# Performance work log

Measured on AMD Instinct MI355X. Metric: run time of the kernel, lower is better.

## Reference

```python
import jax, jax.numpy as jnp
import numpy as np

EPS = 1e-5

def _conv3x3(x, w, b):
    y = jax.lax.conv_general_dilated(x, w, window_strides=(1, 1),
                                     padding=((1, 1), (1, 1)),
                                     dimension_numbers=('NCHW', 'OIHW', 'NCHW'))
    return y + b[None, :, None, None]

def _bilinear_gather(x, py, px):
    # x: [B,C,H,W]; py,px: [B,K,H,W] absolute sampling coords; zero outside image (DCN convention).
    B, C, H, W = x.shape
    Kk = py.shape[1]
    y0 = jnp.floor(py)
    x0 = jnp.floor(px)
    ly = py - y0
    lx = px - x0
    y0i = y0.astype(jnp.int32)
    x0i = x0.astype(jnp.int32)
    xf = x.reshape(B, C, H * W)

    def gather(yi, xi):
        valid = (yi >= 0) & (yi < H) & (xi >= 0) & (xi < W)
        idx = (jnp.clip(yi, 0, H - 1) * W + jnp.clip(xi, 0, W - 1)).reshape(B, -1)
        g = jax.vmap(lambda xb, ib: xb[:, ib])(xf, idx).reshape(B, C, Kk, H, W)
        return g * valid[:, None].astype(x.dtype)

    v00 = gather(y0i, x0i)
    v01 = gather(y0i, x0i + 1)
    v10 = gather(y0i + 1, x0i)
    v11 = gather(y0i + 1, x0i + 1)
    ly = ly[:, None]
    lx = lx[:, None]
    return (v00 * (1 - ly) * (1 - lx) + v01 * (1 - ly) * lx
            + v10 * ly * (1 - lx) + v11 * ly * lx)

def _shift_forward(x, w_off, b_off, w_conv, b_conv, gamma, beta, run_mean, run_var):
    B, C, H, W = x.shape
    om = _conv3x3(x, w_off, b_off)              # [B,27,H,W] offset/mask predictor
    dy = om[:, 0:18:2]                          # [B,9,H,W] per-tap y offsets
    dx = om[:, 1:18:2]                          # [B,9,H,W] per-tap x offsets
    mask = jax.nn.sigmoid(om[:, 18:27])         # [B,9,H,W] modulation (DCNv2)
    kk = jnp.arange(3, dtype=x.dtype) - 1.0     # kernel tap offsets for 3x3, dilation 1
    ky = jnp.repeat(kk, 3)                      # [9]
    kx = jnp.tile(kk, 3)                        # [9]
    hh = jnp.arange(H, dtype=x.dtype)
    ww = jnp.arange(W, dtype=x.dtype)
    py = hh[None, None, :, None] + ky[None, :, None, None] + dy
    px = ww[None, None, None, :] + kx[None, :, None, None] + dx
    s = _bilinear_gather(x, py, px) * mask[:, None]   # [B,C,9,H,W]
    Co = w_conv.shape[0]
    y = jnp.einsum('bckhw,ock->bohw', s, w_conv.reshape(Co, C, 9))
    y = y + b_conv[None, :, None, None]
    # BatchNorm2d (inference) + ReLU, then residual add
    inv = jax.lax.rsqrt(run_var + EPS)
    y = (y - run_mean[None, :, None, None]) * (inv * gamma)[None, :, None, None] + beta[None, :, None, None]
    y = jax.nn.relu(y)
    return x + y

def setup_inputs():
    key = jax.random.key(0)
    ks = jax.random.split(key, 3)
    B, C, H, W = 2, 256, 96, 96
    x = jax.random.normal(ks[0], (B, C, H, W), dtype=jnp.float32)
    w_off = jax.random.normal(ks[1], (27, C, 3, 3), dtype=jnp.float32) * 0.01
    b_off = jnp.zeros((27,), dtype=jnp.float32)
    w_conv = jax.random.normal(ks[2], (C, C, 3, 3), dtype=jnp.float32) * 0.02
    b_conv = jnp.zeros((C,), dtype=jnp.float32)
    gamma = jnp.ones((C,), dtype=jnp.float32)
    beta = jnp.zeros((C,), dtype=jnp.float32)
    run_mean = jnp.zeros((C,), dtype=jnp.float32)
    run_var = jnp.ones((C,), dtype=jnp.float32)
    return {"x": x, "w_off": w_off, "b_off": b_off, "w_conv": w_conv,
            "b_conv": b_conv, "gamma": gamma, "beta": beta,
            "run_mean": run_mean, "run_var": run_var}

def reference(x, w_off, b_off, w_conv, b_conv, gamma, beta, run_mean, run_var):
    return _shift_forward(x, w_off, b_off, w_conv, b_conv, gamma, beta, run_mean, run_var)
```

## Files before the change

### kernel.cpp

```cpp
#include <hip/hip_runtime.h>
#include <hip/hip_bf16.h>

#define H_ 96
#define W_ 96
#define HW_ 9216
#define C_ 256
#define KO_ 27
#define EPS_ 1e-5f

typedef unsigned short u16;
typedef unsigned short ushort8 __attribute__((ext_vector_type(8)));
typedef unsigned short ushort4v __attribute__((ext_vector_type(4)));
typedef short short8v __attribute__((ext_vector_type(8)));
typedef float float4v __attribute__((ext_vector_type(4)));

__device__ __forceinline__ float b2f(u16 u) {
    return __uint_as_float(((unsigned int)u) << 16);
}
__device__ __forceinline__ u16 f2b(float f) {
    __hip_bfloat16 h = __float2bfloat16(f);
    union { __hip_bfloat16 h; u16 u; } cv; cv.h = h; return cv.u;
}
__device__ __forceinline__ unsigned int pack2(float a, float b) {
    union { __hip_bfloat162 h; unsigned int u; } cv;
    cv.h = __float22bfloat162_rn(make_float2(a, b));
    return cv.u;
}
__device__ __forceinline__ void glds16(const u16* g, u16* l) {
    __builtin_amdgcn_global_load_lds(
        (const __attribute__((address_space(1))) void*)g,
        (__attribute__((address_space(3))) void*)l, 16, 0, 0);
}

__global__ __launch_bounds__(256) void prep_kernel(
    const float* __restrict__ x,
    const float* __restrict__ w_conv, const float* __restrict__ w_off,
    const float* __restrict__ b_conv,
    const float* __restrict__ gamma, const float* __restrict__ beta,
    const float* __restrict__ rmean, const float* __restrict__ rvar,
    float* __restrict__ AB, u16* __restrict__ WQ, u16* __restrict__ WO,
    u16* __restrict__ XT)
{
    __shared__ __align__(16) u16 sbuf[32][264];
    const int bx = blockIdx.x;
    const int tid = threadIdx.x;

    if (bx < 576) {
        const int seg = bx % 3, hh = (bx / 3) % 96, bb = bx / 288;
        const int w0s = seg * 32;
        {
            const int c = tid;
            const float* xp = x + ((bb * C_ + c) * H_ + hh) * W_ + w0s;
            float4 xv[8];
#pragma unroll
            for (int j = 0; j < 8; j++) xv[j] = *(const float4*)(xp + j * 4);
#pragma unroll
            for (int j = 0; j < 8; j++) {
                sbuf[j * 4 + 0][c] = f2b(xv[j].x);
                sbuf[j * 4 + 1][c] = f2b(xv[j].y);
                sbuf[j * 4 + 2][c] = f2b(xv[j].z);
                sbuf[j * 4 + 3][c] = f2b(xv[j].w);
            }
        }
        __syncthreads();
#pragma unroll
        for (int it = 0; it < 4; ++it) {
            int u = it * 256 + tid;
            int px = u >> 5, slot = u & 31;
            ushort8 v = *(const ushort8*)&sbuf[px][slot * 8];
            *(ushort8*)&XT[((bb * H_ + hh) * W_ + w0s + px) * C_ + slot * 8] = v;
        }
    } else if (bx < 832) {
        int o = bx - 576;
        u16* flat = &sbuf[0][0];
        for (int i = tid; i < 2304; i += 256)
            flat[i] = f2b(w_conv[o * 2304 + i]);
        __syncthreads();
        int cg = tid >> 5, ln = tid & 31;
#pragma unroll
        for (int k = 0; k < 9; ++k)
            WQ[(k * 8 + cg) * 8192 + o * 32 + ln] = flat[(cg * 32 + ln) * 9 + k];
    } else if (bx < 864) {
        int o = bx - 832;
        u16* flat = &sbuf[0][0];
        for (int i = tid; i < 2304; i += 256)
            flat[i] = (o < KO_) ? f2b(w_off[o * 2304 + i]) : (u16)0;
        __syncthreads();
        int cg = tid >> 5, ln = tid & 31;
#pragma unroll
        for (int k = 0; k < 9; ++k)
            WO[(k * 8 + cg) * 1024 + o * 32 + ln] = flat[(cg * 32 + ln) * 9 + k];
    } else {
        int o = tid;
        float sc = gamma[o] * rsqrtf(rvar[o] + EPS_);
        AB[o] = sc;
        AB[256 + o] = beta[o] + (b_conv[o] - rmean[o]) * sc;
    }
}

__global__ __launch_bounds__(256) void fused_kernel(
    const float* __restrict__ x, const u16* __restrict__ XT,
    const u16* __restrict__ WO, const float* __restrict__ b_off,
    const u16* __restrict__ WQ, const float* __restrict__ AB,
    float* __restrict__ out)
{
    __shared__ __align__(16) unsigned char smem[40960];
    u16*   sA   = (u16*)smem;
    u16*   sB   = (u16*)(smem + 32768);
    float* offv = (float*)(smem + 36864);
    float (*red)[2][32][17] = (float (*)[2][32][17])smem;

    const int tid  = threadIdx.x;
    const int wave = tid >> 6;
    const int lane = tid & 63;
    const int quad = lane >> 4;
    const int l15  = lane & 15;

    const int bid = blockIdx.x;
    const int swz = (bid & 7) * 72 + (bid >> 3);
    const int n0  = swz * 32;
    const int b   = n0 / HW_;
    const int p0  = n0 - b * HW_;
    const int h   = p0 / W_;
    const int w0  = p0 % W_;

    {
        float4v oa[2][2];
#pragma unroll
        for (int ph = 0; ph < 2; ph++)
#pragma unroll
            for (int hh = 0; hh < 2; hh++)
                oa[ph][hh] = float4v{0.f, 0.f, 0.f, 0.f};

        int basec0 = 0, basec1 = 0; bool vld0 = true, vld1 = true;
        auto oset = [&](int tap) {
            int py = h + tap / 3 - 1;
            bool vy = (unsigned)py < (unsigned)H_;
            int pyc = min(max(py, 0), H_ - 1);
            int rowb = (b * H_ + pyc) * W_;
            {
                int pxl = w0 + l15 + tap % 3 - 1;
                vld0 = vy && ((unsigned)pxl < (unsigned)W_);
                basec0 = (rowb + min(max(pxl, 0), W_ - 1)) * C_ + quad * 8;
            }
            {
                int pxl = w0 + 16 + l15 + tap % 3 - 1;
                vld1 = vy && ((unsigned)pxl < (unsigned)W_);
                basec1 = (rowb + min(max(pxl, 0), W_ - 1)) * C_ + quad * 8;
            }
        };
        auto bld0 = [&](int c32) -> ushort8 {
            ushort8 v = *(const ushort8*)(XT + basec0 + (c32 & 7) * 32);
#pragma unroll
            for (int j = 0; j < 8; j++) v[j] = vld0 ? v[j] : (u16)0;
            return v;
        };
        auto bld1 = [&](int c32) -> ushort8 {
            ushort8 v = *(const ushort8*)(XT + basec1 + (c32 & 7) * 32);
#pragma unroll
            for (int j = 0; j < 8; j++) v[j] = vld1 ? v[j] : (u16)0;
            return v;
        };
        const int i0 = wave * 18, i1 = i0 + 18;
        int curtap = i0 >> 3;
        oset(curtap);
        ushort8 b0 = bld0(i0), b1 = bld1(i0);
        short8v wa = *(const short8v*)(WO + i0 * 1024 + l15 * 32 + quad * 8);
        short8v wb = *(const short8v*)(WO + i0 * 1024 + l15 * 32 + quad * 8 + 512);
        for (int i = i0; i < i1; ++i) {
            ushort8 c0v = b0, c1v = b1;
            short8v wac = wa, wbc = wb;
            int nx = i + 1;
            if (nx < i1) {
                int t = nx >> 3;
                if (t != curtap) { oset(t); curtap = t; }
                b0 = bld0(nx); b1 = bld1(nx);
                wa = *(const short8v*)(WO + nx * 1024 + l15 * 32 + quad * 8);
                wb = *(const short8v*)(WO + nx * 1024 + l15 * 32 + quad * 8 + 512);
            }
            union { ushort8 u; short8v s; } u0, u1; u0.u = c0v; u1.u = c1v;
            oa[0][0] = __builtin_amdgcn_mfma_f32_16x16x32_bf16(wac, u0.s, oa[0][0], 0, 0, 0);
            oa[0][1] = __builtin_amdgcn_mfma_f32_16x16x32_bf16(wbc, u0.s, oa[0][1], 0, 0, 0);
            oa[1][0] = __builtin_amdgcn_mfma_f32_16x16x32_bf16(wac, u1.s, oa[1][0], 0, 0, 0);
            oa[1][1] = __builtin_amdgcn_mfma_f32_16x16x32_bf16(wbc, u1.s, oa[1][1], 0, 0, 0);
        }
#pragma unroll
        for (int r = 0; r < 4; ++r) {
            red[wave][0][quad * 4 + r][l15]      = oa[0][0][r];
            red[wave][0][16 + quad * 4 + r][l15] = oa[0][1][r];
            red[wave][1][quad * 4 + r][l15]      = oa[1][0][r];
            red[wave][1][16 + quad * 4 + r][l15] = oa[1][1][r];
        }
    }
    __syncthreads();
    for (int u = tid; u < 1024; u += 256) {
        int px = u & 31, o = u >> 5;
        if (o < KO_) {
            int ph = px >> 4, pp = px & 15;
            float v = red[0][ph][o][pp] + red[1][ph][o][pp]
                    + red[2][ph][o][pp] + red[3][ph][o][pp] + b_off[o];
            offv[px * 32 + o] = (o < 18) ? v : 1.f / (1.f + expf(-v));
        }
    }
    __syncthreads();

    float4v acc[4][2];
#pragma unroll
    for (int i = 0; i < 4; i++)
#pragma unroll
        for (int jj = 0; jj < 2; jj++)
            acc[i][jj] = float4v{0.f, 0.f, 0.f, 0.f};

    const int le8 = lane * 8;
    const int wo  = wave * 64;

    const int ppx = tid >> 3;
    const int pj  = tid & 7;
    const int sboff = (pj >> 2) * 1024 + ppx * 32 + (pj & 3) * 8;

    float fc0, fc1, fc2, fc3, fn0, fn1, fn2, fn3;
    int a00, a01, a10, a11;

    auto tap_setup = [&](int tap) {
        float dy = offv[ppx * 32 + 2 * tap];
        float dx = offv[ppx * 32 + 2 * tap + 1];
        float m  = offv[ppx * 32 + 18 + tap];
        float py  = (float)(h + tap / 3 - 1) + dy;
        float pxx = (float)(w0 + ppx + tap % 3 - 1) + dx;
        float y0f = floorf(py), x0f = floorf(pxx);
        float ly = py - y0f, lx = pxx - x0f;
        int y0 = (int)y0f, x0i = (int)x0f;
        int y1 = y0 + 1, x1 = x0i + 1;
        bool vy0 = (unsigned)y0 < (unsigned)H_;
        bool vy1 = (unsigned)y1 < (unsigned)H_;
        bool vx0 = (unsigned)x0i < (unsigned)W_;
        bool vx1 = (unsigned)x1 < (unsigned)W_;
        fn0 = (vy0 && vx0) ? (1.f - ly) * (1.f - lx) * m : 0.f;
        fn1 = (vy0 && vx1) ? (1.f - ly) * lx * m : 0.f;
        fn2 = (vy1 && vx0) ? ly * (1.f - lx) * m : 0.f;
        fn3 = (vy1 && vx1) ? ly * lx * m : 0.f;
        int y0c = min(max(y0, 0), H_ - 1), y1c = min(max(y1, 0), H_ - 1);
        int x0c = min(max(x0i, 0), W_ - 1), x1c = min(max(x1, 0), W_ - 1);
        a00 = ((b * H_ + y0c) * W_ + x0c) * C_;
        a01 = ((b * H_ + y0c) * W_ + x1c) * C_;
        a10 = ((b * H_ + y1c) * W_ + x0c) * C_;
        a11 = ((b * H_ + y1c) * W_ + x1c) * C_;
    };
    auto stageA = [&](int tap, int q) {
#pragma unroll
        for (int i = 0; i < 8; ++i) {
            int unit = i * 4 + wave;
            int cc = unit >> 4;
            glds16(WQ + (size_t)(tap * 8 + q * 2 + cc) * 8192
                      + (unit & 15) * 512 + le8,
                   &sA[unit * 512]);
        }
    };

    tap_setup(0);
    fc0 = fn0; fc1 = fn1; fc2 = fn2; fc3 = fn3;
    ushort8 gc00 = *(const ushort8*)(XT + a00 + pj * 8);
    ushort8 gc01 = *(const ushort8*)(XT + a01 + pj * 8);
    ushort8 gc10 = *(const ushort8*)(XT + a10 + pj * 8);
    ushort8 gc11 = *(const ushort8*)(XT + a11 + pj * 8);
    stageA(0, 0);
    ushort8 gn00{}, gn01{}, gn10{}, gn11{};

#pragma unroll 4
    for (int ch = 0; ch < 36; ++ch) {
        {
            float v[8];
#pragma unroll
            for (int t = 0; t < 8; t++)
                v[t] = fc0 * b2f(gc00[t]) + fc1 * b2f(gc01[t])
                     + fc2 * b2f(gc10[t]) + fc3 * b2f(gc11[t]);
            uint4 sv;
            sv.x = pack2(v[0], v[1]);
            sv.y = pack2(v[2], v[3]);
            sv.z = pack2(v[4], v[5]);
            sv.w = pack2(v[6], v[7]);
            *(uint4*)&sB[sboff] = sv;
        }
        asm volatile("s_waitcnt vmcnt(0) lgkmcnt(0)" ::: "memory");
        __builtin_amdgcn_s_barrier();

        short8v af[2][4], bfr[2][2];
#pragma unroll
        for (int cc = 0; cc < 2; ++cc) {
#pragma unroll
            for (int mt = 0; mt < 4; ++mt)
                af[cc][mt] = *(const short8v*)
                    &sA[cc * 8192 + (wo + mt * 16 + l15) * 32 + quad * 8];
#pragma unroll
            for (int nt = 0; nt < 2; ++nt)
                bfr[cc][nt] = *(const short8v*)
                    &sB[cc * 1024 + (nt * 16 + l15) * 32 + quad * 8];
        }
        asm volatile("s_waitcnt lgkmcnt(0)" ::: "memory");
        __builtin_amdgcn_s_barrier();

        if (ch < 35) {
            const int chn = ch + 1, tapn = chn >> 2, qn = chn & 3;
            if (qn == 0) tap_setup(tapn);
            const int cb = qn * 64 + pj * 8;
            gn00 = *(const ushort8*)(XT + a00 + cb);
            gn01 = *(const ushort8*)(XT + a01 + cb);
            gn10 = *(const ushort8*)(XT + a10 + cb);
            gn11 = *(const ushort8*)(XT + a11 + cb);
            stageA(tapn, qn);
        }
        __builtin_amdgcn_s_setprio(1);
#pragma unroll
        for (int cc = 0; cc < 2; ++cc)
#pragma unroll
            for (int mt = 0; mt < 4; ++mt)
#pragma unroll
                for (int nt = 0; nt < 2; ++nt)
                    acc[mt][nt] = __builtin_amdgcn_mfma_f32_16x16x32_bf16(
                        af[cc][mt], bfr[cc][nt], acc[mt][nt], 0, 0, 0);
        __builtin_amdgcn_s_setprio(0);
        gc00 = gn00; gc01 = gn01; gc10 = gn10; gc11 = gn11;
        fc0 = fn0; fc1 = fn1; fc2 = fn2; fc3 = fn3;
    }

    const float* Ao = AB;
    const float* Bo = AB + 256;
#pragma unroll
    for (int mt = 0; mt < 4; mt++) {
#pragma unroll
        for (int nt = 0; nt < 2; nt++) {
            int pix = p0 + nt * 16 + l15;
#pragma unroll
            for (int r = 0; r < 4; r++) {
                int o = wo + mt * 16 + quad * 4 + r;
                float v = acc[mt][nt][r] * Ao[o] + Bo[o];
                v = fmaxf(v, 0.f);
                int gi = (b * C_ + o) * HW_ + pix;
                out[gi] = x[gi] + v;
            }
        }
    }
}

extern "C" void kernel_launch(void* const* d_in, const int* in_sizes, int n_in,
                              void* d_out, int out_size, void* d_ws, size_t ws_size,
                              hipStream_t stream)
{
    (void)in_sizes; (void)n_in; (void)out_size; (void)ws_size;
    const float* x      = (const float*)d_in[0];
    const float* w_off  = (const float*)d_in[1];
    const float* b_off  = (const float*)d_in[2];
    const float* w_conv = (const float*)d_in[3];
    const float* b_conv = (const float*)d_in[4];
    const float* gamma  = (const float*)d_in[5];
    const float* beta   = (const float*)d_in[6];
    const float* rmean  = (const float*)d_in[7];
    const float* rvar   = (const float*)d_in[8];
    float* out = (float*)d_out;

    float* ws = (float*)d_ws;
    float* AB = ws;
    u16* WQ = (u16*)(AB + 512);
    u16* WO = WQ + 589824;
    u16* XT = WO + 73728;

    prep_kernel<<<865, 256, 0, stream>>>(x, w_conv, w_off, b_conv, gamma, beta,
                                         rmean, rvar, AB, WQ, WO, XT);
    fused_kernel<<<576, 256, 0, stream>>>(x, XT, WO, b_off, WQ, AB, out);
}
```

Measured before the change: 172.4 us.

## Halve pixel tile per block to 16 and double the grid

Each block now handles 16 pixels instead of 32, so the grid doubles from 576 to 1152 blocks. The offset-predictor MFMAs, the reduction buffer and the B tile shrink to match, and only half the threads produce the bilinear samples. This is meant to fill more of the GPU's compute units and cut the per-block tail. In exchange, every weight tile (WQ, WO) is now loaded twice as often for the same output, and each MFMA gets half the B reuse, which raises weight bandwidth and per-block overhead.

```diff
diff --git a/kernel.cpp b/kernel.cpp
--- a/kernel.cpp
+++ b/kernel.cpp
@@ -104,11 +104,11 @@
     const u16* __restrict__ WQ, const float* __restrict__ AB,
     float* __restrict__ out)
 {
-    __shared__ __align__(16) unsigned char smem[40960];
+    __shared__ __align__(16) unsigned char smem[36864];
     u16*   sA   = (u16*)smem;
     u16*   sB   = (u16*)(smem + 32768);
-    float* offv = (float*)(smem + 36864);
-    float (*red)[2][32][17] = (float (*)[2][32][17])smem;
+    float* offv = (float*)(smem + 34816);
+    float (*red)[32][17] = (float (*)[32][17])smem;
 
     const int tid  = threadIdx.x;
     const int wave = tid >> 6;
@@ -117,106 +117,85 @@
     const int l15  = lane & 15;
 
     const int bid = blockIdx.x;
-    const int swz = (bid & 7) * 72 + (bid >> 3);
-    const int n0  = swz * 32;
+    const int swz = (bid & 7) * 144 + (bid >> 3);
+    const int n0  = swz * 16;
     const int b   = n0 / HW_;
     const int p0  = n0 - b * HW_;
     const int h   = p0 / W_;
     const int w0  = p0 % W_;
 
     {
-        float4v oa[2][2];
-#pragma unroll
-        for (int ph = 0; ph < 2; ph++)
-#pragma unroll
-            for (int hh = 0; hh < 2; hh++)
-                oa[ph][hh] = float4v{0.f, 0.f, 0.f, 0.f};
-
-        int basec0 = 0, basec1 = 0; bool vld0 = true, vld1 = true;
+        float4v oa0 = float4v{0.f, 0.f, 0.f, 0.f};
+        float4v oa1 = float4v{0.f, 0.f, 0.f, 0.f};
+
+        int basec = 0; bool vld = true;
         auto oset = [&](int tap) {
             int py = h + tap / 3 - 1;
             bool vy = (unsigned)py < (unsigned)H_;
             int pyc = min(max(py, 0), H_ - 1);
             int rowb = (b * H_ + pyc) * W_;
-            {
-                int pxl = w0 + l15 + tap % 3 - 1;
-                vld0 = vy && ((unsigned)pxl < (unsigned)W_);
-                basec0 = (rowb + min(max(pxl, 0), W_ - 1)) * C_ + quad * 8;
-            }
-            {
-                int pxl = w0 + 16 + l15 + tap % 3 - 1;
-                vld1 = vy && ((unsigned)pxl < (unsigned)W_);
-                basec1 = (rowb + min(max(pxl, 0), W_ - 1)) * C_ + quad * 8;
-            }
+            int pxl = w0 + l15 + tap % 3 - 1;
+            vld = vy && ((unsigned)pxl < (unsigned)W_);
+            basec = (rowb + min(max(pxl, 0), W_ - 1)) * C_ + quad * 8;
         };
-        auto bld0 = [&](int c32) -> ushort8 {
-            ushort8 v = *(const ushort8*)(XT + basec0 + (c32 & 7) * 32);
-#pragma unroll
-            for (int j = 0; j < 8; j++) v[j] = vld0 ? v[j] : (u16)0;
-            return v;
-        };
-        auto bld1 = [&](int c32) -> ushort8 {
-            ushort8 v = *(const ushort8*)(XT + basec1 + (c32 & 7) * 32);
-#pragma unroll
-            for (int j = 0; j < 8; j++) v[j] = vld1 ? v[j] : (u16)0;
+        auto bld = [&](int c32) -> ushort8 {
+            ushort8 v = *(const ushort8*)(XT + basec + (c32 & 7) * 32);
+#pragma unroll
+            for (int j = 0; j < 8; j++) v[j] = vld ? v[j] : (u16)0;
             return v;
         };
         const int i0 = wave * 18, i1 = i0 + 18;
         int curtap = i0 >> 3;
         oset(curtap);
-        ushort8 b0 = bld0(i0), b1 = bld1(i0);
+        ushort8 b0 = bld(i0);
         short8v wa = *(const short8v*)(WO + i0 * 1024 + l15 * 32 + quad * 8);
         short8v wb = *(const short8v*)(WO + i0 * 1024 + l15 * 32 + quad * 8 + 512);
         for (int i = i0; i < i1; ++i) {
-            ushort8 c0v = b0, c1v = b1;
+            ushort8 c0v = b0;
             short8v wac = wa, wbc = wb;
             int nx = i + 1;
             if (nx < i1) {
                 int t = nx >> 3;
                 if (t != curtap) { oset(t); curtap = t; }
-                b0 = bld0(nx); b1 = bld1(nx);
+                b0 = bld(nx);
                 wa = *(const short8v*)(WO + nx * 1024 + l15 * 32 + quad * 8);
                 wb = *(const short8v*)(WO + nx * 1024 + l15 * 32 + quad * 8 + 512);
             }
-            union { ushort8 u; short8v s; } u0, u1; u0.u = c0v; u1.u = c1v;
-            oa[0][0] = __builtin_amdgcn_mfma_f32_16x16x32_bf16(wac, u0.s, oa[0][0], 0, 0, 0);
-            oa[0][1] = __builtin_amdgcn_mfma_f32_16x16x32_bf16(wbc, u0.s, oa[0][1], 0, 0, 0);
-            oa[1][0] = __builtin_amdgcn_mfma_f32_16x16x32_bf16(wac, u1.s, oa[1][0], 0, 0, 0);
-            oa[1][1] = __builtin_amdgcn_mfma_f32_16x16x32_bf16(wbc, u1.s, oa[1][1], 0, 0, 0);
+            union { ushort8 u; short8v s; } u0; u0.u = c0v;
+            oa0 = __builtin_amdgcn_mfma_f32_16x16x32_bf16(wac, u0.s, oa0, 0, 0, 0);
+            oa1 = __builtin_amdgcn_mfma_f32_16x16x32_bf16(wbc, u0.s, oa1, 0, 0, 0);
         }
 #pragma unroll
         for (int r = 0; r < 4; ++r) {
-            red[wave][0][quad * 4 + r][l15]      = oa[0][0][r];
-            red[wave][0][16 + quad * 4 + r][l15] = oa[0][1][r];
-            red[wave][1][quad * 4 + r][l15]      = oa[1][0][r];
-            red[wave][1][16 + quad * 4 + r][l15] = oa[1][1][r];
+            red[wave][quad * 4 + r][l15]      = oa0[r];
+            red[wave][16 + quad * 4 + r][l15] = oa1[r];
         }
     }
     __syncthreads();
-    for (int u = tid; u < 1024; u += 256) {
-        int px = u & 31, o = u >> 5;
+#pragma unroll
+    for (int rep = 0; rep < 2; ++rep) {
+        int u = rep * 256 + tid;
+        int o = u >> 4, px = u & 15;
         if (o < KO_) {
-            int ph = px >> 4, pp = px & 15;
-            float v = red[0][ph][o][pp] + red[1][ph][o][pp]
-                    + red[2][ph][o][pp] + red[3][ph][o][pp] + b_off[o];
+            float v = red[0][o][px] + red[1][o][px]
+                    + red[2][o][px] + red[3][o][px] + b_off[o];
             offv[px * 32 + o] = (o < 18) ? v : 1.f / (1.f + expf(-v));
         }
     }
     __syncthreads();
 
-    float4v acc[4][2];
+    float4v acc[4];
 #pragma unroll
     for (int i = 0; i < 4; i++)
-#pragma unroll
-        for (int jj = 0; jj < 2; jj++)
-            acc[i][jj] = float4v{0.f, 0.f, 0.f, 0.f};
+        acc[i] = float4v{0.f, 0.f, 0.f, 0.f};
 
     const int le8 = lane * 8;
     const int wo  = wave * 64;
 
-    const int ppx = tid >> 3;
+    const bool prod = tid < 128;
+    const int ppx = (tid >> 3) & 15;
     const int pj  = tid & 7;
-    const int sboff = (pj >> 2) * 1024 + ppx * 32 + (pj & 3) * 8;
+    const int sboff = (pj >> 2) * 512 + ppx * 32 + (pj & 3) * 8;
 
     float fc0, fc1, fc2, fc3, fn0, fn1, fn2, fn3;
     int a00, a01, a10, a11;
@@ -259,16 +238,19 @@
 
     tap_setup(0);
     fc0 = fn0; fc1 = fn1; fc2 = fn2; fc3 = fn3;
-    ushort8 gc00 = *(const ushort8*)(XT + a00 + pj * 8);
-    ushort8 gc01 = *(const ushort8*)(XT + a01 + pj * 8);
-    ushort8 gc10 = *(const ushort8*)(XT + a10 + pj * 8);
-    ushort8 gc11 = *(const ushort8*)(XT + a11 + pj * 8);
+    ushort8 gc00{}, gc01{}, gc10{}, gc11{};
+    if (prod) {
+        gc00 = *(const ushort8*)(XT + a00 + pj * 8);
+        gc01 = *(const ushort8*)(XT + a01 + pj * 8);
+        gc10 = *(const ushort8*)(XT + a10 + pj * 8);
+        gc11 = *(const ushort8*)(XT + a11 + pj * 8);
+    }
     stageA(0, 0);
     ushort8 gn00{}, gn01{}, gn10{}, gn11{};
 
 #pragma unroll 4
     for (int ch = 0; ch < 36; ++ch) {
-        {
+        if (prod) {
             float v[8];
 #pragma unroll
             for (int t = 0; t < 8; t++)
@@ -284,17 +266,15 @@
         asm volatile("s_waitcnt vmcnt(0) lgkmcnt(0)" ::: "memory");
         __builtin_amdgcn_s_barrier();
 
-        short8v af[2][4], bfr[2][2];
+        short8v af[2][4], bfr[2];
 #pragma unroll
         for (int cc = 0; cc < 2; ++cc) {
 #pragma unroll
             for (int mt = 0; mt < 4; ++mt)
                 af[cc][mt] = *(const short8v*)
                     &sA[cc * 8192 + (wo + mt * 16 + l15) * 32 + quad * 8];
-#pragma unroll
-            for (int nt = 0; nt < 2; ++nt)
-                bfr[cc][nt] = *(const short8v*)
-                    &sB[cc * 1024 + (nt * 16 + l15) * 32 + quad * 8];
+            bfr[cc] = *(const short8v*)
+                    &sB[cc * 512 + l15 * 32 + quad * 8];
         }
         asm volatile("s_waitcnt lgkmcnt(0)" ::: "memory");
         __builtin_amdgcn_s_barrier();
@@ -302,11 +282,13 @@
         if (ch < 35) {
             const int chn = ch + 1, tapn = chn >> 2, qn = chn & 3;
             if (qn == 0) tap_setup(tapn);
-            const int cb = qn * 64 + pj * 8;
-            gn00 = *(const ushort8*)(XT + a00 + cb);
-            gn01 = *(const ushort8*)(XT + a01 + cb);
-            gn10 = *(const ushort8*)(XT + a10 + cb);
-            gn11 = *(const ushort8*)(XT + a11 + cb);
+            if (prod) {
+                const int cb = qn * 64 + pj * 8;
+                gn00 = *(const ushort8*)(XT + a00 + cb);
+                gn01 = *(const ushort8*)(XT + a01 + cb);
+                gn10 = *(const ushort8*)(XT + a10 + cb);
+                gn11 = *(const ushort8*)(XT + a11 + cb);
+            }
             stageA(tapn, qn);
         }
         __builtin_amdgcn_s_setprio(1);
@@ -314,10 +296,8 @@
         for (int cc = 0; cc < 2; ++cc)
 #pragma unroll
             for (int mt = 0; mt < 4; ++mt)
-#pragma unroll
-                for (int nt = 0; nt < 2; ++nt)
-                    acc[mt][nt] = __builtin_amdgcn_mfma_f32_16x16x32_bf16(
-                        af[cc][mt], bfr[cc][nt], acc[mt][nt], 0, 0, 0);
+                acc[mt] = __builtin_amdgcn_mfma_f32_16x16x32_bf16(
+                    af[cc][mt], bfr[cc], acc[mt], 0, 0, 0);
         __builtin_amdgcn_s_setprio(0);
         gc00 = gn00; gc01 = gn01; gc10 = gn10; gc11 = gn11;
         fc0 = fn0; fc1 = fn1; fc2 = fn2; fc3 = fn3;
@@ -325,19 +305,16 @@
 
     const float* Ao = AB;
     const float* Bo = AB + 256;
+    const int pix = p0 + l15;
 #pragma unroll
     for (int mt = 0; mt < 4; mt++) {
 #pragma unroll
-        for (int nt = 0; nt < 2; nt++) {
-            int pix = p0 + nt * 16 + l15;
-#pragma unroll
-            for (int r = 0; r < 4; r++) {
-                int o = wo + mt * 16 + quad * 4 + r;
-                float v = acc[mt][nt][r] * Ao[o] + Bo[o];
-                v = fmaxf(v, 0.f);
-                int gi = (b * C_ + o) * HW_ + pix;
-                out[gi] = x[gi] + v;
-            }
+        for (int r = 0; r < 4; r++) {
+            int o = wo + mt * 16 + quad * 4 + r;
+            float v = acc[mt][r] * Ao[o] + Bo[o];
+            v = fmaxf(v, 0.f);
+            int gi = (b * C_ + o) * HW_ + pix;
+            out[gi] = x[gi] + v;
         }
     }
 }
@@ -366,5 +343,5 @@
 
     prep_kernel<<<865, 256, 0, stream>>>(x, w_conv, w_off, b_conv, gamma, beta,
                                          rmean, rvar, AB, WQ, WO, XT);
-    fused_kernel<<<576, 256, 0, stream>>>(x, XT, WO, b_off, WQ, AB, out);
-}
+    fused_kernel<<<1152, 256, 0, stream>>>(x, XT, WO, b_off, WQ, AB, out);
+}
```

Result: slower. 197.5 us (+14.5%).
